# Kernel tuning notes

Hardware: AMD Instinct MI355X
Metric: run time of the kernel (lower is better)

The kernel has to match this reference:

```python
import jax, jax.numpy as jnp
import numpy as np

WS = 8          # window_size
NH = 8          # num_heads
D = 256         # values_dim
DQK = 128       # inner_qk_dim = int(256 * 0.5)
DV = 256        # inner_v_dim (already divisible by NH)
H1, W1 = 128, 128
H2, W2 = 192, 192
N1 = (H1 // WS) * (W1 // WS)   # 256 windows
N2 = (H2 // WS) * (W2 // WS)   # 576 windows
EPS = 1e-6


def _windows(x):
    # (B, H, W, D) -> (B, Wh*Ww, ws*ws, D)
    B, Hx, Wx, Dd = x.shape
    Wh, Ww = Hx // WS, Wx // WS
    x = x.reshape(B, Wh, WS, Ww, WS, Dd).transpose(0, 1, 3, 2, 4, 5)
    return x.reshape(B, Wh * Ww, WS * WS, Dd), (Wh, Ww)


def _unwindows(x, Wh, Ww):
    # (B, Wh*Ww, ws*ws, D) -> (B, Wh*ws, Ww*ws, D)
    B, N, n, Dd = x.shape
    x = x.reshape(B, Wh, Ww, WS, WS, Dd).transpose(0, 1, 3, 2, 4, 5)
    return x.reshape(B, Wh * WS, Ww * WS, Dd)


def _rmsnorm(x, w):
    return x * jax.lax.rsqrt(jnp.mean(x * x, axis=-1, keepdims=True) + EPS) * w


def _qkv(x, W_qk, b_qk, rms_w, W_v):
    Vw, (Wh, Ww) = _windows(x)
    B, N, n, _ = Vw.shape
    avg = Vw.mean(axis=2)                                  # (B, N, D)
    qk = _rmsnorm(avg @ W_qk + b_qk, rms_w)                # (B, N, 2*DQK)
    # 'b Wh Ww (H e) -> b H (Wh Ww) e' then chunk(2, dim=-1)
    qk = qk.reshape(B, N, NH, 2 * DQK // NH).transpose(0, 2, 1, 3)  # (B, NH, N, 32)
    q, k = jnp.split(qk, 2, axis=-1)                       # each (B, NH, N, 16)
    v = Vw @ W_v                                           # (B, N, n, DV)
    ev = DV // NH
    # 'b Wh Ww n (e H) -> b H (Wh Ww) (n e)' (head index fastest-varying in channel)
    v = v.reshape(B, N, n, ev, NH).transpose(0, 4, 1, 2, 3).reshape(B, NH, N, n * ev)
    return q, k, v, (Wh, Ww)


def reference(x1, x2, W_qk, b_qk, rms_w, W_v, W_vb):
    q1, k1, v1, s1 = _qkv(x1, W_qk, b_qk, rms_w, W_v)
    q2, k2, v2, s2 = _qkv(x2, W_qk, b_qk, rms_w, W_v)
    q = jnp.concatenate([q1, q2], axis=2)   # (B, NH, N, 16)
    k = jnp.concatenate([k1, k2], axis=2)
    v = jnp.concatenate([v1, v2], axis=2)   # (B, NH, N, n*ev)

    scale = 1.0 / jnp.sqrt(jnp.asarray(DQK, dtype=q.dtype))
    scores = jnp.einsum('bhqe,bhke->bhqk', q, k) * scale   # (B, NH, N, N)
    # block-diagonal self-source mask
    src_id = jnp.concatenate([jnp.zeros((N1,), jnp.int32), jnp.ones((N2,), jnp.int32)])
    mask = src_id[:, None] == src_id[None, :]              # (N, N) True within same source
    scores = jnp.where(mask, -jnp.inf, scores)
    A = jax.nn.softmax(scores, axis=-1)

    out = jnp.einsum('bhqk,bhkf->bhqf', A, v)              # (B, NH, N, n*ev)
    B = out.shape[0]
    n = WS * WS
    ev = DV // NH
    N = N1 + N2
    # 'b H N (n e) -> b N n (e H)'
    out = out.reshape(B, NH, N, n, ev).transpose(0, 2, 3, 4, 1).reshape(B, N, n, ev * NH)
    out = out @ W_vb                                       # (B, N, n, D)

    o1 = _unwindows(out[:, :N1], H1 // WS, W1 // WS)
    o2 = _unwindows(out[:, N1:], H2 // WS, W2 // WS)
    return (o1, o2)


def setup_inputs() -> dict:
    key = jax.random.key(0)
    ks = jax.random.split(key, 6)
    return {
        'x1': jax.random.normal(ks[0], (2, H1, W1, D), jnp.float32),
        'x2': jax.random.normal(ks[1], (2, H2, W2, D), jnp.float32),
        'W_qk': jax.random.normal(ks[2], (D, 2 * DQK), jnp.float32) * 0.02,
        'b_qk': jnp.zeros((2 * DQK,), jnp.float32),
        'rms_w': jnp.ones((2 * DQK,), jnp.float32),
        'W_v': jax.random.normal(ks[3], (D, DV), jnp.float32) * 0.02,
        'W_vb': jax.random.normal(ks[4], (DV, D), jnp.float32) * 0.02,
    }
```

## Files before the change

### kernel.cpp

```cpp
#include <hip/hip_runtime.h>

typedef __attribute__((ext_vector_type(8))) short bf16x8;
typedef __attribute__((ext_vector_type(4))) float f32x4;

#define NWIN 832
#define N1_ 256
#define N2_ 576
#define O1SZ 8388608

__device__ __forceinline__ ushort f2bf(float f) {
    union { float f; unsigned u; } v; v.f = f;
    unsigned r = v.u + 0x7fffu + ((v.u >> 16) & 1u);
    return (ushort)(r >> 16);
}

__global__ __launch_bounds__(256) void k_prep(const float* __restrict__ W_qk,
        const float* __restrict__ W_v, const float* __restrict__ W_vb,
        ushort* __restrict__ WvT, ushort* __restrict__ WvbT, float* __restrict__ WqkT)
{
    int row = blockIdx.x & 255, m = blockIdx.x >> 8, t = threadIdx.x;
    if (m == 0) {
        int j = ((row & 31) << 3) | (row >> 5);
        WvT[row * 256 + t] = f2bf(W_v[t * 256 + j]);
    } else if (m == 1) {
        WvbT[row * 256 + t] = f2bf(W_vb[t * 256 + row]);
    } else {
        WqkT[row * 256 + t] = W_qk[t * 256 + row];
    }
}

__global__ __launch_bounds__(256) void k_projv(const float* __restrict__ x1, const float* __restrict__ x2,
        const ushort* __restrict__ WvT, float* __restrict__ avg, ushort* __restrict__ vattn)
{
    __shared__ ushort a_lds[64][264];
    int bid = blockIdx.x, b = bid / NWIN, win = bid % NWIN;
    const float* src; int Wd, base;
    if (win < N1_) { src = x1; Wd = 128; int wh = win >> 4, ww = win & 15;
                     base = ((b*128 + wh*8)*128 + ww*8)*256; }
    else           { src = x2; Wd = 192; int w2 = win - N1_; int wh = w2/24, ww = w2%24;
                     base = ((b*192 + wh*8)*192 + ww*8)*256; }
    int c = threadIdx.x;
    float s = 0.f;
    #pragma unroll 8
    for (int i = 0; i < 64; ++i) {
        float g = src[base + ((i>>3)*Wd + (i&7))*256 + c];
        s += g;
        a_lds[i][c] = f2bf(g);
    }
    avg[(b*NWIN + win)*256 + c] = s * 0.015625f;
    __syncthreads();

    int lane = threadIdx.x & 63, wv = threadIdx.x >> 6;
    int lr = lane & 15, lg = lane >> 4;
    f32x4 acc[4][4];
    #pragma unroll
    for (int mt=0;mt<4;++mt)
      #pragma unroll
      for (int nt=0;nt<4;++nt) acc[mt][nt] = (f32x4){0.f,0.f,0.f,0.f};

    #pragma unroll 2
    for (int ks = 0; ks < 8; ++ks) {
        bf16x8 af[4], bfr[4];
        #pragma unroll
        for (int mt=0;mt<4;++mt) af[mt] = *(const bf16x8*)&a_lds[mt*16 + lr][ks*32 + lg*8];
        #pragma unroll
        for (int nt=0;nt<4;++nt) bfr[nt] = *(const bf16x8*)&WvT[(wv*64 + nt*16 + lr)*256 + ks*32 + lg*8];
        #pragma unroll
        for (int mt=0;mt<4;++mt)
          #pragma unroll
          for (int nt=0;nt<4;++nt)
            acc[mt][nt] = __builtin_amdgcn_mfma_f32_16x16x32_bf16(af[mt], bfr[nt], acc[mt][nt], 0, 0, 0);
    }
    #pragma unroll
    for (int nt=0;nt<4;++nt) {
        int ncol = wv*64 + nt*16 + lr, h = ncol >> 5, e = ncol & 31;
        ushort* pb = &vattn[((size_t)(b*8 + h)*NWIN + win)*2048 + e];
        #pragma unroll
        for (int mt=0;mt<4;++mt)
          #pragma unroll
          for (int r=0;r<4;++r) {
            int i = mt*16 + lg*4 + r;
            pb[i*32] = f2bf(acc[mt][nt][r]);
          }
    }
}

__global__ __launch_bounds__(256) void k_qk(const float* __restrict__ avg, const float* __restrict__ WqkT,
        const float* __restrict__ b_qk, const float* __restrict__ rms_w,
        float* __restrict__ qv, float* __restrict__ kv)
{
    __shared__ float arow[256];
    __shared__ float red[256];
    int row = blockIdx.x, c = threadIdx.x;
    arow[c] = avg[row*256 + c];
    __syncthreads();
    const float4* wr = (const float4*)&WqkT[c*256];
    float t = 0.f;
    #pragma unroll 8
    for (int k4 = 0; k4 < 64; ++k4) {
        float4 w = wr[k4];
        t += arow[k4*4]*w.x + arow[k4*4+1]*w.y + arow[k4*4+2]*w.z + arow[k4*4+3]*w.w;
    }
    t += b_qk[c];
    red[c] = t*t;
    __syncthreads();
    for (int s = 128; s; s >>= 1) { if (c < s) red[c] += red[c+s]; __syncthreads(); }
    float ms = red[0] * (1.f/256.f);
    float y = t * rsqrtf(ms + 1e-6f) * rms_w[c];
    int b = row / NWIN, win = row % NWIN;
    int h = c >> 5, sub = c & 31;
    size_t ob = ((size_t)(b*8 + h)*NWIN + win)*16 + (sub & 15);
    if (sub < 16) qv[ob] = y; else kv[ob] = y;
}

__global__ __launch_bounds__(256) void k_sm(const float* __restrict__ qv, const float* __restrict__ kv,
        ushort* __restrict__ Amat)
{
    __shared__ float red[256];
    int rowid = blockIdx.x;
    int qg = rowid % NWIN, bh = rowid / NWIN;
    bool s1 = qg < N1_;
    int Nk = s1 ? N2_ : N1_;
    int kbase = s1 ? N1_ : 0;
    size_t Abase = (size_t)bh*294912 + (s1 ? (size_t)qg*576 : (147456 + (size_t)(qg - N1_)*256));
    const float4* qp = (const float4*)&qv[((size_t)bh*NWIN + qg)*16];
    float4 q0 = qp[0], q1 = qp[1], q2 = qp[2], q3 = qp[3];
    const float* kp = &kv[((size_t)bh*NWIN + kbase)*16];
    int t = threadIdx.x;
    float sc[3];
    #pragma unroll
    for (int it = 0; it < 3; ++it) {
        int kk = t + it*256;
        sc[it] = -1e30f;
        if (kk < Nk) {
            const float4* kr = (const float4*)&kp[(size_t)kk*16];
            float4 a = kr[0], bq = kr[1], cq = kr[2], dq = kr[3];
            float d = q0.x*a.x + q0.y*a.y + q0.z*a.z + q0.w*a.w
                    + q1.x*bq.x + q1.y*bq.y + q1.z*bq.z + q1.w*bq.w
                    + q2.x*cq.x + q2.y*cq.y + q2.z*cq.z + q2.w*cq.w
                    + q3.x*dq.x + q3.y*dq.y + q3.z*dq.z + q3.w*dq.w;
            sc[it] = d * 0.08838834764831845f;
        }
    }
    float m = fmaxf(fmaxf(sc[0], sc[1]), sc[2]);
    red[t] = m; __syncthreads();
    for (int s = 128; s; s >>= 1) { if (t < s) red[t] = fmaxf(red[t], red[t+s]); __syncthreads(); }
    float M = red[0];
    __syncthreads();
    float e0 = __expf(sc[0]-M), e1 = __expf(sc[1]-M), e2 = __expf(sc[2]-M);
    red[t] = e0 + e1 + e2; __syncthreads();
    for (int s = 128; s; s >>= 1) { if (t < s) red[t] += red[t+s]; __syncthreads(); }
    float inv = 1.f / red[0];
    float ex[3] = {e0, e1, e2};
    #pragma unroll
    for (int it = 0; it < 3; ++it) {
        int kk = t + it*256;
        if (kk < Nk) Amat[Abase + kk] = f2bf(ex[it]*inv);
    }
}

__global__ __launch_bounds__(256) void k_av(const ushort* __restrict__ Amat,
        const ushort* __restrict__ vattn, ushort* __restrict__ outc)
{
    __shared__ ushort a_lds[64][40];
    __shared__ ushort v_lds[256][40];
    int bid = blockIdx.x;
    int bh = bid / 104, r = bid % 104, fc = r / 13, qc = r % 13;
    int Nk, kbase, q0, qg0, Astride; size_t Abase;
    if (qc < 4) { Nk = N2_; kbase = N1_; q0 = qc*64; qg0 = q0;
                  Abase = (size_t)bh*294912 + (size_t)q0*576; Astride = 576; }
    else        { Nk = N1_; kbase = 0; q0 = (qc-4)*64; qg0 = N1_ + q0;
                  Abase = (size_t)bh*294912 + 147456 + (size_t)q0*256; Astride = 256; }
    const ushort* vbase = &vattn[((size_t)bh*NWIN + kbase)*2048 + fc*256];
    int t = threadIdx.x;
    int lane = t & 63, wv = t >> 6, lr = lane & 15, lg = lane >> 4;
    f32x4 acc[4][4];
    #pragma unroll
    for (int mt=0;mt<4;++mt)
      #pragma unroll
      for (int nt=0;nt<4;++nt) acc[mt][nt] = (f32x4){0.f,0.f,0.f,0.f};

    int nsteps = Nk >> 5;
    for (int ks = 0; ks < nsteps; ++ks) {
        __syncthreads();
        {
            int q = t >> 2, seg = t & 3;
            const ushort* gp = &Amat[Abase + (size_t)q*Astride + ks*32 + seg*8];
            *(uint4*)&a_lds[q][seg*8] = *(const uint4*)gp;
        }
        {
            int krow = t >> 3, u = t & 7;
            int kw = krow ^ ((u & 3) << 3);
            const ushort* vp = &vbase[(size_t)(ks*32 + krow)*2048];
            #pragma unroll
            for (int j = 0; j < 4; ++j) {
                int f0 = (u + 8*j) * 8;
                uint4 d = *(const uint4*)&vp[f0];
                const ushort* dv = (const ushort*)&d;
                #pragma unroll
                for (int jj = 0; jj < 8; ++jj) v_lds[f0 + jj][kw] = dv[jj];
            }
        }
        __syncthreads();
        bf16x8 af[4];
        #pragma unroll
        for (int mt=0;mt<4;++mt) af[mt] = *(const bf16x8*)&a_lds[mt*16 + lr][lg*8];
        #pragma unroll
        for (int nt=0;nt<4;++nt) {
            int f = wv*64 + nt*16 + lr;
            int s3r = (f >> 3) & 3;
            bf16x8 bb = *(const bf16x8*)&v_lds[f][(lg ^ s3r) << 3];
            #pragma unroll
            for (int mt=0;mt<4;++mt)
                acc[mt][nt] = __builtin_amdgcn_mfma_f32_16x16x32_bf16(af[mt], bb, acc[mt][nt], 0, 0, 0);
        }
    }
    size_t ob = ((size_t)bh*NWIN + qg0)*2048 + fc*256;
    #pragma unroll
    for (int nt=0;nt<4;++nt) {
        int f = wv*64 + nt*16 + lr;
        #pragma unroll
        for (int mt=0;mt<4;++mt)
          #pragma unroll
          for (int rr=0;rr<4;++rr) {
            int q = mt*16 + lg*4 + rr;
            outc[ob + (size_t)q*2048 + f] = f2bf(acc[mt][nt][rr]);
          }
    }
}

__global__ __launch_bounds__(256) void k_out(const ushort* __restrict__ outc,
        const ushort* __restrict__ WvbT, float* __restrict__ out)
{
    __shared__ ushort a_lds[64][264];
    int bid = blockIdx.x, b = bid / NWIN, win = bid % NWIN;
    int t = threadIdx.x;
    int i_ = (t*8) >> 5, e0 = (t*8) & 31;
    #pragma unroll
    for (int h = 0; h < 8; ++h) {
        const ushort* pp = &outc[((size_t)(b*8 + h)*NWIN + win)*2048 + t*8];
        uint4 d = *(const uint4*)pp;
        const ushort* dv = (const ushort*)&d;
        #pragma unroll
        for (int jj = 0; jj < 8; ++jj) a_lds[i_][(e0 + jj)*8 + h] = dv[jj];
    }
    __syncthreads();

    int lane = t & 63, wv = t >> 6, lr = lane & 15, lg = lane >> 4;
    f32x4 acc[4][4];
    #pragma unroll
    for (int mt=0;mt<4;++mt)
      #pragma unroll
      for (int nt=0;nt<4;++nt) acc[mt][nt] = (f32x4){0.f,0.f,0.f,0.f};

    #pragma unroll 2
    for (int ks = 0; ks < 8; ++ks) {
        bf16x8 af[4], bfr[4];
        #pragma unroll
        for (int mt=0;mt<4;++mt) af[mt] = *(const bf16x8*)&a_lds[mt*16 + lr][ks*32 + lg*8];
        #pragma unroll
        for (int nt=0;nt<4;++nt) bfr[nt] = *(const bf16x8*)&WvbT[(wv*64 + nt*16 + lr)*256 + ks*32 + lg*8];
        #pragma unroll
        for (int mt=0;mt<4;++mt)
          #pragma unroll
          for (int nt=0;nt<4;++nt)
            acc[mt][nt] = __builtin_amdgcn_mfma_f32_16x16x32_bf16(af[mt], bfr[nt], acc[mt][nt], 0, 0, 0);
    }

    int Wd, base;
    if (win < N1_) { Wd = 128; int wh = win >> 4, ww = win & 15;
                     base = ((b*128 + wh*8)*128 + ww*8)*256; }
    else           { Wd = 192; int w2 = win - N1_; int wh = w2/24, ww = w2%24;
                     base = O1SZ + ((b*192 + wh*8)*192 + ww*8)*256; }
    #pragma unroll
    for (int nt=0;nt<4;++nt) {
        int dcol = wv*64 + nt*16 + lr;
        #pragma unroll
        for (int mt=0;mt<4;++mt)
          #pragma unroll
          for (int rr=0;rr<4;++rr) {
            int i = mt*16 + lg*4 + rr;
            out[base + ((i>>3)*Wd + (i&7))*256 + dcol] = acc[mt][nt][rr];
          }
    }
}

extern "C" void kernel_launch(void* const* d_in, const int* in_sizes, int n_in,
                              void* d_out, int out_size, void* d_ws, size_t ws_size,
                              hipStream_t stream) {
    const float* x1    = (const float*)d_in[0];
    const float* x2    = (const float*)d_in[1];
    const float* W_qk  = (const float*)d_in[2];
    const float* b_qk  = (const float*)d_in[3];
    const float* rms_w = (const float*)d_in[4];
    const float* W_v   = (const float*)d_in[5];
    const float* W_vb  = (const float*)d_in[6];

    char* ws = (char*)d_ws;
    ushort* WvT   = (ushort*)(ws + 0);
    ushort* WvbT  = (ushort*)(ws + 131072);
    float*  WqkT  = (float*) (ws + 262144);
    float*  avg   = (float*) (ws + 524288);
    float*  qv    = (float*) (ws + 2228224);
    float*  kv    = (float*) (ws + 3080192);
    ushort* vattn = (ushort*)(ws + 3932160);
    ushort* Amat  = (ushort*)(ws + 58458112);
    ushort* outc  = (ushort*)(ws + 67895296);

    k_prep <<<768,   256, 0, stream>>>(W_qk, W_v, W_vb, WvT, WvbT, WqkT);
    k_projv<<<1664,  256, 0, stream>>>(x1, x2, WvT, avg, vattn);
    k_qk   <<<1664,  256, 0, stream>>>(avg, WqkT, b_qk, rms_w, qv, kv);
    k_sm   <<<13312, 256, 0, stream>>>(qv, kv, Amat);
    k_av   <<<1664,  256, 0, stream>>>(Amat, vattn, outc);
    k_out  <<<1664,  256, 0, stream>>>(outc, WvbT, (float*)d_out);
}
```

Measured before the change: 422.7 us.

## Coalesce V projection stores via LDS staging and vectorize LDS transposes

k_projv now reads the input window with float4 loads and combines partial column sums through shared memory. It stages the bf16 V results in LDS so each head slice is written to global memory with 16-byte stores, which also changes the per-window V layout from (n,e) to (e,n). The attention V-tile transpose and the k_out gather are reworked to write packed ushort2 and ushort4 elements into LDS, using the new layout. The aim is to replace scattered 2-byte global stores and scalar LDS writes, at the cost of an extra barrier and more shared memory.

After: 410.3 us. -2.9%, faster.

```diff
diff --git a/kernel.cpp b/kernel.cpp
--- a/kernel.cpp
+++ b/kernel.cpp
@@ -32,26 +32,39 @@
 __global__ __launch_bounds__(256) void k_projv(const float* __restrict__ x1, const float* __restrict__ x2,
         const ushort* __restrict__ WvT, float* __restrict__ avg, ushort* __restrict__ vattn)
 {
-    __shared__ ushort a_lds[64][264];
+    __shared__ __align__(16) char smem[37888];
+    ushort (*a_lds)[264] = (ushort (*)[264])smem;
+    float* psumF = (float*)(smem + 33792);
+
     int bid = blockIdx.x, b = bid / NWIN, win = bid % NWIN;
     const float* src; int Wd, base;
     if (win < N1_) { src = x1; Wd = 128; int wh = win >> 4, ww = win & 15;
                      base = ((b*128 + wh*8)*128 + ww*8)*256; }
     else           { src = x2; Wd = 192; int w2 = win - N1_; int wh = w2/24, ww = w2%24;
                      base = ((b*192 + wh*8)*192 + ww*8)*256; }
-    int c = threadIdx.x;
-    float s = 0.f;
-    #pragma unroll 8
-    for (int i = 0; i < 64; ++i) {
-        float g = src[base + ((i>>3)*Wd + (i&7))*256 + c];
-        s += g;
-        a_lds[i][c] = f2bf(g);
-    }
-    avg[(b*NWIN + win)*256 + c] = s * 0.015625f;
-    __syncthreads();
-
-    int lane = threadIdx.x & 63, wv = threadIdx.x >> 6;
-    int lr = lane & 15, lg = lane >> 4;
+
+    int t = threadIdx.x;
+    int c4 = t & 63, tg = t >> 6;
+    int c0 = c4 * 4;
+    const float* sp = src + base + c0;
+    float4 s4 = {0.f, 0.f, 0.f, 0.f};
+    #pragma unroll
+    for (int k = 0; k < 16; ++k) {
+        int i = tg*16 + k;
+        float4 g = *(const float4*)(sp + ((i>>3)*Wd + (i&7))*256);
+        s4.x += g.x; s4.y += g.y; s4.z += g.z; s4.w += g.w;
+        ushort4 hb = { f2bf(g.x), f2bf(g.y), f2bf(g.z), f2bf(g.w) };
+        *(ushort4*)&a_lds[i][c0] = hb;
+    }
+    *(float4*)&psumF[tg*256 + c0] = s4;
+    __syncthreads();
+
+    {
+        float a = psumF[t] + psumF[256 + t] + psumF[512 + t] + psumF[768 + t];
+        avg[(b*NWIN + win)*256 + t] = a * 0.015625f;
+    }
+
+    int lane = t & 63, wv = t >> 6, lr = lane & 15, lg = lane >> 4;
     f32x4 acc[4][4];
     #pragma unroll
     for (int mt=0;mt<4;++mt)
@@ -71,17 +84,30 @@
           for (int nt=0;nt<4;++nt)
             acc[mt][nt] = __builtin_amdgcn_mfma_f32_16x16x32_bf16(af[mt], bfr[nt], acc[mt][nt], 0, 0, 0);
     }
-    #pragma unroll
-    for (int nt=0;nt<4;++nt) {
-        int ncol = wv*64 + nt*16 + lr, h = ncol >> 5, e = ncol & 31;
-        ushort* pb = &vattn[((size_t)(b*8 + h)*NWIN + win)*2048 + e];
-        #pragma unroll
-        for (int mt=0;mt<4;++mt)
-          #pragma unroll
-          for (int r=0;r<4;++r) {
-            int i = mt*16 + lg*4 + r;
-            pb[i*32] = f2bf(acc[mt][nt][r]);
-          }
+
+    __syncthreads();
+    ushort (*sw)[72] = (ushort (*)[72])(smem + wv*9216);
+
+    #pragma unroll
+    for (int nt=0; nt<4; ++nt) {
+        int c = nt*16 + lr;
+        #pragma unroll
+        for (int mt=0; mt<4; ++mt) {
+            ushort4 hb = { f2bf(acc[mt][nt][0]), f2bf(acc[mt][nt][1]),
+                           f2bf(acc[mt][nt][2]), f2bf(acc[mt][nt][3]) };
+            *(ushort4*)&sw[c][mt*16 + lg*4] = hb;
+        }
+    }
+    #pragma unroll
+    for (int u=0; u<2; ++u) {
+        int h = wv*2 + u;
+        ushort* dst = &vattn[((size_t)(b*8 + h)*NWIN + win)*2048];
+        #pragma unroll
+        for (int it=0; it<4; ++it) {
+            int q = it*64 + lane;
+            int e = q >> 3, i8 = (q & 7) * 8;
+            *(uint4*)&dst[e*64 + i8] = *(const uint4*)&sw[u*32 + e][i8];
+        }
     }
 }
 
@@ -189,16 +215,23 @@
             *(uint4*)&a_lds[q][seg*8] = *(const uint4*)gp;
         }
         {
-            int krow = t >> 3, u = t & 7;
-            int kw = krow ^ ((u & 3) << 3);
-            const ushort* vp = &vbase[(size_t)(ks*32 + krow)*2048];
+            int u = t & 7, rp = (t >> 3) & 15, half = t >> 7;
+            int k0 = rp * 2;
+            int kw = k0 ^ ((u & 3) << 3);
+            const ushort* vp0 = &vbase[(size_t)(ks*32 + k0)*2048];
+            const ushort* vp1 = vp0 + 2048;
             #pragma unroll
-            for (int j = 0; j < 4; ++j) {
-                int f0 = (u + 8*j) * 8;
-                uint4 d = *(const uint4*)&vp[f0];
-                const ushort* dv = (const ushort*)&d;
+            for (int j = 0; j < 2; ++j) {
+                int f0 = (u + 8*(half*2 + j)) * 8;
+                uint4 d0 = *(const uint4*)&vp0[f0];
+                uint4 d1 = *(const uint4*)&vp1[f0];
+                const ushort* a0 = (const ushort*)&d0;
+                const ushort* a1 = (const ushort*)&d1;
                 #pragma unroll
-                for (int jj = 0; jj < 8; ++jj) v_lds[f0 + jj][kw] = dv[jj];
+                for (int jj = 0; jj < 8; ++jj) {
+                    ushort2 w2 = { a0[jj], a1[jj] };
+                    *(ushort2*)&v_lds[f0 + jj][kw] = w2;
+                }
             }
         }
         __syncthreads();
@@ -235,14 +268,22 @@
     __shared__ ushort a_lds[64][264];
     int bid = blockIdx.x, b = bid / NWIN, win = bid % NWIN;
     int t = threadIdx.x;
-    int i_ = (t*8) >> 5, e0 = (t*8) & 31;
-    #pragma unroll
-    for (int h = 0; h < 8; ++h) {
-        const ushort* pp = &outc[((size_t)(b*8 + h)*NWIN + win)*2048 + t*8];
-        uint4 d = *(const uint4*)pp;
-        const ushort* dv = (const ushort*)&d;
-        #pragma unroll
-        for (int jj = 0; jj < 8; ++jj) a_lds[i_][(e0 + jj)*8 + h] = dv[jj];
+    int e = t >> 3, i0 = (t & 7) * 8;
+    #pragma unroll
+    for (int hg = 0; hg < 2; ++hg) {
+        uint4 d[4];
+        #pragma unroll
+        for (int hh = 0; hh < 4; ++hh)
+            d[hh] = *(const uint4*)&outc[((size_t)(b*8 + hg*4 + hh)*NWIN + win)*2048 + t*8];
+        const ushort* p0 = (const ushort*)&d[0];
+        const ushort* p1 = (const ushort*)&d[1];
+        const ushort* p2 = (const ushort*)&d[2];
+        const ushort* p3 = (const ushort*)&d[3];
+        #pragma unroll
+        for (int jj = 0; jj < 8; ++jj) {
+            ushort4 w = { p0[jj], p1[jj], p2[jj], p3[jj] };
+            *(ushort4*)&a_lds[i0 + jj][e*8 + hg*4] = w;
+        }
     }
     __syncthreads();
 
```
